# Kernel tuning notes

Hardware: AMD Instinct MI355X
Metric: run time of the kernel (lower is better)

Reference implementation:

```python
import jax, jax.numpy as jnp
import numpy as np

INPUT_DIM = 1024
DAY_EMB = 8
PRED_LEN = 96
HIDDEN = 512
BATCH = 4096


def setup_inputs() -> dict:
    key = jax.random.key(0)
    ks = jax.random.split(key, 6)
    x = jax.random.normal(ks[0], (BATCH, INPUT_DIM), dtype=jnp.float32)
    day_emb = jax.random.normal(ks[1], (PRED_LEN, DAY_EMB), dtype=jnp.float32)
    # stacked per-head first-layer weights: in = input_dim + day_emb_dim
    W1 = jax.random.normal(ks[2], (PRED_LEN, INPUT_DIM + DAY_EMB, HIDDEN), dtype=jnp.float32) * 0.02
    b1 = jax.random.normal(ks[3], (PRED_LEN, HIDDEN), dtype=jnp.float32) * 0.02
    # stacked per-head output Linear(hidden, 1) weights (squeezed)
    W2 = jax.random.normal(ks[4], (PRED_LEN, HIDDEN), dtype=jnp.float32) * 0.02
    b2 = jax.random.normal(ks[5], (PRED_LEN,), dtype=jnp.float32) * 0.02
    return {"x": x, "day_emb": day_emb, "W1": W1, "b1": b1, "W2": W2, "b2": b2}


def reference(x, day_emb, W1, b1, W2, b2):
    # Each head p sees f = concat([x, day_emb[p]]) -> Linear -> ReLU -> (Dropout eval=id) -> Linear(.,1)
    # Split W1 into the x-part and emb-part so we never materialize the [P,B,in+emb] concat.
    W1x = W1[:, :INPUT_DIM, :]          # [P, D, H]
    W1e = W1[:, INPUT_DIM:, :]          # [P, E, H]
    h = jnp.einsum('bd,pdh->pbh', x, W1x)  # [P, B, H]
    h = h + (jnp.einsum('pe,peh->ph', day_emb, W1e) + b1)[:, None, :]
    h = jax.nn.relu(h)
    out = jnp.einsum('pbh,ph->pb', h, W2) + b2[:, None]  # [P, B]
    return out.T  # [B, pred_len]
```

## Files before the change

### kernel.cpp

```cpp
#include <hip/hip_runtime.h>
#include <hip/hip_bf16.h>
#include <stdint.h>

#define INPUT_DIM 1024
#define PRED_LEN 96
#define HIDDEN 512
#define BATCH 4096
#define W1_ROWS 1032

typedef __attribute__((ext_vector_type(8))) short bf16x8;
typedef __attribute__((ext_vector_type(4))) float floatx4;

__device__ __forceinline__ unsigned short f32_to_bf16_rne(float f) {
    union { float f; unsigned int u; } v; v.f = f;
    unsigned int u = v.u;
    unsigned int r = u + 0x7fffu + ((u >> 16) & 1u);
    return (unsigned short)(r >> 16);
}

__device__ __forceinline__ void async_copy16(const void* g, void* l) {
    __builtin_amdgcn_global_load_lds(
        (const __attribute__((address_space(1))) unsigned int*)g,
        (__attribute__((address_space(3))) unsigned int*)l, 16, 0, 0);
}

__global__ void convert_x_kernel(const float* __restrict__ x,
                                 unsigned short* __restrict__ xb) {
    int i = (blockIdx.x * 256 + threadIdx.x) * 4;
    float4 v = *reinterpret_cast<const float4*>(x + i);
    ushort4 o;
    o.x = f32_to_bf16_rne(v.x);
    o.y = f32_to_bf16_rne(v.y);
    o.z = f32_to_bf16_rne(v.z);
    o.w = f32_to_bf16_rne(v.w);
    *reinterpret_cast<ushort4*>(xb + i) = o;
}

__global__ void transpose_w1_kernel(const float* __restrict__ W1,
                                    unsigned short* __restrict__ W1t) {
    __shared__ unsigned short tile[64 * 64];
    int bid = blockIdx.x;
    int nt = bid & 7;
    int kt = (bid >> 3) & 15;
    int p  = bid >> 7;
    int t  = threadIdx.x;
    const float* src = W1 + (size_t)p * W1_ROWS * HIDDEN;
    const int k0 = kt * 64, n0 = nt * 64;

    const int tn = t & 15;
    const int tk = t >> 4;
    float4 v[4];
    #pragma unroll
    for (int i = 0; i < 4; ++i)
        v[i] = *reinterpret_cast<const float4*>(src + (size_t)(k0 + 4 * tk + i) * HIDDEN + n0 + 4 * tn);
    const int slot1 = ((tk >> 2) ^ (tn & 3)) * 16 + (tk & 3) * 4;
    {
        ushort4 w0, w1, w2, w3;
        w0.x = f32_to_bf16_rne(v[0].x); w0.y = f32_to_bf16_rne(v[1].x);
        w0.z = f32_to_bf16_rne(v[2].x); w0.w = f32_to_bf16_rne(v[3].x);
        w1.x = f32_to_bf16_rne(v[0].y); w1.y = f32_to_bf16_rne(v[1].y);
        w1.z = f32_to_bf16_rne(v[2].y); w1.w = f32_to_bf16_rne(v[3].y);
        w2.x = f32_to_bf16_rne(v[0].z); w2.y = f32_to_bf16_rne(v[1].z);
        w2.z = f32_to_bf16_rne(v[2].z); w2.w = f32_to_bf16_rne(v[3].z);
        w3.x = f32_to_bf16_rne(v[0].w); w3.y = f32_to_bf16_rne(v[1].w);
        w3.z = f32_to_bf16_rne(v[2].w); w3.w = f32_to_bf16_rne(v[3].w);
        *reinterpret_cast<ushort4*>(tile + (4 * tn + 0) * 64 + slot1) = w0;
        *reinterpret_cast<ushort4*>(tile + (4 * tn + 1) * 64 + slot1) = w1;
        *reinterpret_cast<ushort4*>(tile + (4 * tn + 2) * 64 + slot1) = w2;
        *reinterpret_cast<ushort4*>(tile + (4 * tn + 3) * 64 + slot1) = w3;
    }
    __syncthreads();

    const int nr = t >> 2;
    const int q  = t & 3;
    const int slot2 = (q ^ ((nr >> 2) & 3)) * 16;
    uint4 a = *reinterpret_cast<const uint4*>(tile + nr * 64 + slot2);
    uint4 b = *reinterpret_cast<const uint4*>(tile + nr * 64 + slot2 + 8);
    size_t dst = ((size_t)p * HIDDEN + n0 + nr) * 1024 + k0 + q * 16;
    *reinterpret_cast<uint4*>(W1t + dst)     = a;
    *reinterpret_cast<uint4*>(W1t + dst + 8) = b;
}

__global__ void bias_kernel(const float* __restrict__ W1,
                            const float* __restrict__ day_emb,
                            const float* __restrict__ b1,
                            float* __restrict__ bias) {
    int p = blockIdx.x;
    int h = threadIdx.x;
    const float* W1e = W1 + ((size_t)p * W1_ROWS + INPUT_DIM) * HIDDEN;
    float acc = b1[p * HIDDEN + h];
    #pragma unroll
    for (int e = 0; e < 8; ++e)
        acc += day_emb[p * 8 + e] * W1e[(size_t)e * HIDDEN + h];
    bias[p * HIDDEN + h] = acc;
}

__global__ void __launch_bounds__(512, 2)
mlp_head_kernel(const unsigned short* __restrict__ xb,
                const unsigned short* __restrict__ W1t,
                const float* __restrict__ bias,
                const float* __restrict__ W2,
                const float* __restrict__ b2,
                float* __restrict__ out)
{
    __shared__ unsigned short A_lds[2][256 * 64];
    __shared__ unsigned short B_lds[2][256 * 64];
    __shared__ float w2s[HIDDEN];
    __shared__ float biass[HIDDEN];
    __shared__ float red[4][256];

    const int mt   = blockIdx.x;
    const int p    = blockIdx.y;
    const int t    = threadIdx.x;
    const int lane = t & 63;
    const int w    = t >> 6;
    const int wm   = w >> 2;
    const int wn   = w & 3;
    const int l15  = lane & 15;
    const int quad = lane >> 4;
    const int sl0  = (quad ^ (l15 & 7)) * 8;
    const int sl1  = ((4 + quad) ^ (l15 & 7)) * 8;

    const int aro = (wm * 128 + l15) * 64;
    const int bro = (wn * 64  + l15) * 64;

    const int tr   = t >> 3;
    const int skc  = ((t & 7) ^ (tr & 7)) * 8;
    const int ldst = t * 8;

    const int m0 = mt * 256;
    const unsigned short* agb = xb  + (size_t)(m0 + tr) * 1024 + skc;
    const unsigned short* bgb = W1t + ((size_t)p * HIDDEN + tr) * 1024 + skc;

    for (int i = t; i < HIDDEN; i += 512) {
        w2s[i]   = W2[p * HIDDEN + i];
        biass[i] = bias[p * HIDDEN + i];
    }
    __syncthreads();

    float partial[8][4];
    #pragma unroll
    for (int i = 0; i < 8; ++i)
        #pragma unroll
        for (int r = 0; r < 4; ++r) partial[i][r] = 0.f;

    for (int nt = 0; nt < 2; ++nt) {
        const size_t bnt = (size_t)nt * 256 * 1024;

        floatx4 acc[8][4];
        #pragma unroll
        for (int i = 0; i < 8; ++i)
            #pragma unroll
            for (int j = 0; j < 4; ++j)
                acc[i][j] = (floatx4){0.f, 0.f, 0.f, 0.f};

        #pragma unroll
        for (int part = 0; part < 4; ++part) {
            async_copy16(agb + (size_t)part * 65536,       &A_lds[0][part * 4096 + ldst]);
            async_copy16(bgb + bnt + (size_t)part * 65536, &B_lds[0][part * 4096 + ldst]);
        }
        asm volatile("s_waitcnt vmcnt(0)" ::: "memory");
        __builtin_amdgcn_s_barrier();

        for (int kt = 0; kt < 16; ++kt) {
            const int cur = kt & 1;
            const unsigned short* Ab = A_lds[cur];
            const unsigned short* Bb = B_lds[cur];
            unsigned short* An = A_lds[cur ^ 1];
            unsigned short* Bn = B_lds[cur ^ 1];
            const int kof = (kt + 1) * 64;
            bf16x8 af[4][2], bf[2][2];

            #pragma unroll
            for (int i = 0; i < 4; ++i) {
                af[i][0] = *reinterpret_cast<const bf16x8*>(Ab + aro + i * 1024 + sl0);
                af[i][1] = *reinterpret_cast<const bf16x8*>(Ab + aro + i * 1024 + sl1);
            }
            #pragma unroll
            for (int j = 0; j < 2; ++j) {
                bf[j][0] = *reinterpret_cast<const bf16x8*>(Bb + bro + j * 1024 + sl0);
                bf[j][1] = *reinterpret_cast<const bf16x8*>(Bb + bro + j * 1024 + sl1);
            }
            if (kt < 15) {
                async_copy16(agb + kof,                &An[ldst]);
                async_copy16(agb + 65536 + kof,        &An[4096 + ldst]);
                async_copy16(bgb + bnt + kof,          &Bn[ldst]);
                async_copy16(bgb + bnt + 65536 + kof,  &Bn[4096 + ldst]);
            }
            __builtin_amdgcn_s_barrier();
            __builtin_amdgcn_s_setprio(1);
            #pragma unroll
            for (int i = 0; i < 4; ++i)
                #pragma unroll
                for (int j = 0; j < 2; ++j) {
                    acc[i][j] = __builtin_amdgcn_mfma_f32_16x16x32_bf16(af[i][0], bf[j][0], acc[i][j], 0, 0, 0);
                    acc[i][j] = __builtin_amdgcn_mfma_f32_16x16x32_bf16(af[i][1], bf[j][1], acc[i][j], 0, 0, 0);
                }
            __builtin_amdgcn_s_setprio(0);
            __builtin_amdgcn_s_barrier();

            #pragma unroll
            for (int j = 0; j < 2; ++j) {
                bf[j][0] = *reinterpret_cast<const bf16x8*>(Bb + bro + (j + 2) * 1024 + sl0);
                bf[j][1] = *reinterpret_cast<const bf16x8*>(Bb + bro + (j + 2) * 1024 + sl1);
            }
            if (kt < 15) {
                async_copy16(agb + 131072 + kof,       &An[8192 + ldst]);
                async_copy16(agb + 196608 + kof,       &An[12288 + ldst]);
                async_copy16(bgb + bnt + 131072 + kof, &Bn[8192 + ldst]);
                async_copy16(bgb + bnt + 196608 + kof, &Bn[12288 + ldst]);
            }
            __builtin_amdgcn_s_barrier();
            __builtin_amdgcn_s_setprio(1);
            #pragma unroll
            for (int i = 0; i < 4; ++i)
                #pragma unroll
                for (int j = 0; j < 2; ++j) {
                    acc[i][j + 2] = __builtin_amdgcn_mfma_f32_16x16x32_bf16(af[i][0], bf[j][0], acc[i][j + 2], 0, 0, 0);
                    acc[i][j + 2] = __builtin_amdgcn_mfma_f32_16x16x32_bf16(af[i][1], bf[j][1], acc[i][j + 2], 0, 0, 0);
                }
            __builtin_amdgcn_s_setprio(0);
            __builtin_amdgcn_s_barrier();

            #pragma unroll
            for (int i = 0; i < 4; ++i) {
                af[i][0] = *reinterpret_cast<const bf16x8*>(Ab + aro + (i + 4) * 1024 + sl0);
                af[i][1] = *reinterpret_cast<const bf16x8*>(Ab + aro + (i + 4) * 1024 + sl1);
            }
            __builtin_amdgcn_s_barrier();
            __builtin_amdgcn_s_setprio(1);
            #pragma unroll
            for (int i = 0; i < 4; ++i)
                #pragma unroll
                for (int j = 0; j < 2; ++j) {
                    acc[i + 4][j + 2] = __builtin_amdgcn_mfma_f32_16x16x32_bf16(af[i][0], bf[j][0], acc[i + 4][j + 2], 0, 0, 0);
                    acc[i + 4][j + 2] = __builtin_amdgcn_mfma_f32_16x16x32_bf16(af[i][1], bf[j][1], acc[i + 4][j + 2], 0, 0, 0);
                }
            __builtin_amdgcn_s_setprio(0);
            __builtin_amdgcn_s_barrier();

            #pragma unroll
            for (int j = 0; j < 2; ++j) {
                bf[j][0] = *reinterpret_cast<const bf16x8*>(Bb + bro + j * 1024 + sl0);
                bf[j][1] = *reinterpret_cast<const bf16x8*>(Bb + bro + j * 1024 + sl1);
            }
            __builtin_amdgcn_s_barrier();
            __builtin_amdgcn_s_setprio(1);
            #pragma unroll
            for (int i = 0; i < 4; ++i)
                #pragma unroll
                for (int j = 0; j < 2; ++j) {
                    acc[i + 4][j] = __builtin_amdgcn_mfma_f32_16x16x32_bf16(af[i][0], bf[j][0], acc[i + 4][j], 0, 0, 0);
                    acc[i + 4][j] = __builtin_amdgcn_mfma_f32_16x16x32_bf16(af[i][1], bf[j][1], acc[i + 4][j], 0, 0, 0);
                }
            __builtin_amdgcn_s_setprio(0);
            if (kt < 15)
                asm volatile("s_waitcnt vmcnt(0)" ::: "memory");
            __builtin_amdgcn_s_barrier();
        }

        const int nb0 = nt * 256;
        #pragma unroll
        for (int j = 0; j < 4; ++j) {
            int c = nb0 + wn * 64 + j * 16 + l15;
            float w2v = w2s[c];
            float bv  = biass[c];
            #pragma unroll
            for (int i = 0; i < 8; ++i)
                #pragma unroll
                for (int r = 0; r < 4; ++r) {
                    float hv = acc[i][j][r] + bv;
                    hv = hv > 0.f ? hv : 0.f;
                    partial[i][r] += hv * w2v;
                }
        }
    }

    #pragma unroll
    for (int i = 0; i < 8; ++i)
        #pragma unroll
        for (int r = 0; r < 4; ++r) {
            float v = partial[i][r];
            v += __shfl_xor(v, 1);
            v += __shfl_xor(v, 2);
            v += __shfl_xor(v, 4);
            v += __shfl_xor(v, 8);
            partial[i][r] = v;
        }

    if (l15 == 0) {
        #pragma unroll
        for (int i = 0; i < 8; ++i)
            #pragma unroll
            for (int r = 0; r < 4; ++r) {
                int row = wm * 128 + i * 16 + quad * 4 + r;
                red[wn][row] = partial[i][r];
            }
    }
    __syncthreads();
    if (t < 256) {
        float v = red[0][t] + red[1][t] + red[2][t] + red[3][t] + b2[p];
        out[(size_t)(m0 + t) * PRED_LEN + p] = v;
    }
}

extern "C" void kernel_launch(void* const* d_in, const int* in_sizes, int n_in,
                              void* d_out, int out_size, void* d_ws, size_t ws_size,
                              hipStream_t stream) {
    const float* x       = (const float*)d_in[0];
    const float* day_emb = (const float*)d_in[1];
    const float* W1      = (const float*)d_in[2];
    const float* b1      = (const float*)d_in[3];
    const float* W2      = (const float*)d_in[4];
    const float* b2      = (const float*)d_in[5];
    float* out = (float*)d_out;

    const size_t xb_bytes  = (size_t)BATCH * INPUT_DIM * 2;
    const size_t w1t_bytes = (size_t)PRED_LEN * HIDDEN * INPUT_DIM * 2;
    const size_t bias_bytes = (size_t)PRED_LEN * HIDDEN * 4;
    if (ws_size < xb_bytes + w1t_bytes + bias_bytes) return;

    unsigned short* xb  = (unsigned short*)d_ws;
    unsigned short* w1t = (unsigned short*)((char*)d_ws + xb_bytes);
    float* biasp        = (float*)((char*)d_ws + xb_bytes + w1t_bytes);

    convert_x_kernel<<<(BATCH * INPUT_DIM) / (256 * 4), 256, 0, stream>>>(x, xb);
    transpose_w1_kernel<<<PRED_LEN * 16 * 8, 256, 0, stream>>>(W1, w1t);
    bias_kernel<<<PRED_LEN, HIDDEN, 0, stream>>>(W1, day_emb, b1, biasp);

    dim3 grid(BATCH / 256, PRED_LEN);
    mlp_head_kernel<<<grid, 512, 0, stream>>>(xb, w1t, biasp, W2, b2, out);
}
```

Before: 676.4 us.

## Halve M tile and use triple-buffered LDS pipeline with fused N-tile loop

Shrinks the per-block M tile from 256 to 128 rows, doubling the grid, and replaces the double-buffered, barrier-heavy K loop with a three-stage ring that prefetches two K-steps ahead and waits with a partial vmcnt. The two N halves are merged into one 32-step virtual loop, and the ReLU/W2 epilogue for the first half runs mid-loop. The intent is fewer barriers, deeper load/compute overlap and better occupancy from lower register use. The cost is more total global traffic for W1 tiles, since each W1 panel is now read by twice as many blocks, and the early w2s/bias __syncthreads is removed, so correctness depends on the loop's barrier ordering those shared writes.

```diff
diff --git a/kernel.cpp b/kernel.cpp
--- a/kernel.cpp
+++ b/kernel.cpp
@@ -103,11 +103,11 @@
                 const float* __restrict__ b2,
                 float* __restrict__ out)
 {
-    __shared__ unsigned short A_lds[2][256 * 64];
-    __shared__ unsigned short B_lds[2][256 * 64];
+    __shared__ unsigned short A_lds[3][128 * 64];
+    __shared__ unsigned short B_lds[3][256 * 64];
     __shared__ float w2s[HIDDEN];
     __shared__ float biass[HIDDEN];
-    __shared__ float red[4][256];
+    __shared__ float red[4][128];
 
     const int mt   = blockIdx.x;
     const int p    = blockIdx.y;
@@ -121,14 +121,14 @@
     const int sl0  = (quad ^ (l15 & 7)) * 8;
     const int sl1  = ((4 + quad) ^ (l15 & 7)) * 8;
 
-    const int aro = (wm * 128 + l15) * 64;
-    const int bro = (wn * 64  + l15) * 64;
+    const int aro = (wm * 64 + l15) * 64;
+    const int bro = (wn * 64 + l15) * 64;
 
     const int tr   = t >> 3;
     const int skc  = ((t & 7) ^ (tr & 7)) * 8;
     const int ldst = t * 8;
 
-    const int m0 = mt * 256;
+    const int m0 = mt * 128;
     const unsigned short* agb = xb  + (size_t)(m0 + tr) * 1024 + skc;
     const unsigned short* bgb = W1t + ((size_t)p * HIDDEN + tr) * 1024 + skc;
 
@@ -136,41 +136,63 @@
         w2s[i]   = W2[p * HIDDEN + i];
         biass[i] = bias[p * HIDDEN + i];
     }
-    __syncthreads();
-
-    float partial[8][4];
-    #pragma unroll
-    for (int i = 0; i < 8; ++i)
+
+    float partial[4][4];
+    #pragma unroll
+    for (int i = 0; i < 4; ++i)
         #pragma unroll
         for (int r = 0; r < 4; ++r) partial[i][r] = 0.f;
 
-    for (int nt = 0; nt < 2; ++nt) {
-        const size_t bnt = (size_t)nt * 256 * 1024;
-
-        floatx4 acc[8][4];
-        #pragma unroll
-        for (int i = 0; i < 8; ++i)
-            #pragma unroll
-            for (int j = 0; j < 4; ++j)
-                acc[i][j] = (floatx4){0.f, 0.f, 0.f, 0.f};
-
-        #pragma unroll
-        for (int part = 0; part < 4; ++part) {
-            async_copy16(agb + (size_t)part * 65536,       &A_lds[0][part * 4096 + ldst]);
-            async_copy16(bgb + bnt + (size_t)part * 65536, &B_lds[0][part * 4096 + ldst]);
-        }
-        asm volatile("s_waitcnt vmcnt(0)" ::: "memory");
+    floatx4 acc[4][4];
+    #pragma unroll
+    for (int i = 0; i < 4; ++i)
+        #pragma unroll
+        for (int j = 0; j < 4; ++j)
+            acc[i][j] = (floatx4){0.f, 0.f, 0.f, 0.f};
+
+    {
+        async_copy16(agb,                 &A_lds[0][ldst]);
+        async_copy16(agb + 65536,         &A_lds[0][4096 + ldst]);
+        async_copy16(bgb,                 &B_lds[0][ldst]);
+        async_copy16(bgb + 65536,         &B_lds[0][4096 + ldst]);
+        async_copy16(bgb + 131072,        &B_lds[0][8192 + ldst]);
+        async_copy16(bgb + 196608,        &B_lds[0][12288 + ldst]);
+        async_copy16(agb + 64,            &A_lds[1][ldst]);
+        async_copy16(agb + 65536 + 64,    &A_lds[1][4096 + ldst]);
+        async_copy16(bgb + 64,            &B_lds[1][ldst]);
+        async_copy16(bgb + 65536 + 64,    &B_lds[1][4096 + ldst]);
+        async_copy16(bgb + 131072 + 64,   &B_lds[1][8192 + ldst]);
+        async_copy16(bgb + 196608 + 64,   &B_lds[1][12288 + ldst]);
+    }
+
+    int cs = 0;
+    int ss = 2;
+
+    #pragma unroll 1
+    for (int vkt = 0; vkt < 31; ++vkt) {
+        asm volatile("s_waitcnt vmcnt(6)" ::: "memory");
         __builtin_amdgcn_s_barrier();
 
-        for (int kt = 0; kt < 16; ++kt) {
-            const int cur = kt & 1;
-            const unsigned short* Ab = A_lds[cur];
-            const unsigned short* Bb = B_lds[cur];
-            unsigned short* An = A_lds[cur ^ 1];
-            unsigned short* Bn = B_lds[cur ^ 1];
-            const int kof = (kt + 1) * 64;
+        if (vkt < 30) {
+            const int v2 = vkt + 2;
+            const int ko = (v2 & 15) << 6;
+            const size_t no = (size_t)(v2 >> 4) * 262144;
+            const unsigned short* a2 = agb + ko;
+            const unsigned short* bq = bgb + no + ko;
+            unsigned short* Ad = &A_lds[ss][ldst];
+            unsigned short* Bd = &B_lds[ss][ldst];
+            async_copy16(a2,           Ad);
+            async_copy16(a2 + 65536,   Ad + 4096);
+            async_copy16(bq,           Bd);
+            async_copy16(bq + 65536,   Bd + 4096);
+            async_copy16(bq + 131072,  Bd + 8192);
+            async_copy16(bq + 196608,  Bd + 12288);
+        }
+
+        {
+            const unsigned short* Ab = &A_lds[cs][0];
+            const unsigned short* Bb = &B_lds[cs][0];
             bf16x8 af[4][2], bf[2][2];
-
             #pragma unroll
             for (int i = 0; i < 4; ++i) {
                 af[i][0] = *reinterpret_cast<const bf16x8*>(Ab + aro + i * 1024 + sl0);
@@ -181,13 +203,6 @@
                 bf[j][0] = *reinterpret_cast<const bf16x8*>(Bb + bro + j * 1024 + sl0);
                 bf[j][1] = *reinterpret_cast<const bf16x8*>(Bb + bro + j * 1024 + sl1);
             }
-            if (kt < 15) {
-                async_copy16(agb + kof,                &An[ldst]);
-                async_copy16(agb + 65536 + kof,        &An[4096 + ldst]);
-                async_copy16(bgb + bnt + kof,          &Bn[ldst]);
-                async_copy16(bgb + bnt + 65536 + kof,  &Bn[4096 + ldst]);
-            }
-            __builtin_amdgcn_s_barrier();
             __builtin_amdgcn_s_setprio(1);
             #pragma unroll
             for (int i = 0; i < 4; ++i)
@@ -197,20 +212,11 @@
                     acc[i][j] = __builtin_amdgcn_mfma_f32_16x16x32_bf16(af[i][1], bf[j][1], acc[i][j], 0, 0, 0);
                 }
             __builtin_amdgcn_s_setprio(0);
-            __builtin_amdgcn_s_barrier();
-
             #pragma unroll
             for (int j = 0; j < 2; ++j) {
                 bf[j][0] = *reinterpret_cast<const bf16x8*>(Bb + bro + (j + 2) * 1024 + sl0);
                 bf[j][1] = *reinterpret_cast<const bf16x8*>(Bb + bro + (j + 2) * 1024 + sl1);
             }
-            if (kt < 15) {
-                async_copy16(agb + 131072 + kof,       &An[8192 + ldst]);
-                async_copy16(agb + 196608 + kof,       &An[12288 + ldst]);
-                async_copy16(bgb + bnt + 131072 + kof, &Bn[8192 + ldst]);
-                async_copy16(bgb + bnt + 196608 + kof, &Bn[12288 + ldst]);
-            }
-            __builtin_amdgcn_s_barrier();
             __builtin_amdgcn_s_setprio(1);
             #pragma unroll
             for (int i = 0; i < 4; ++i)
@@ -220,64 +226,83 @@
                     acc[i][j + 2] = __builtin_amdgcn_mfma_f32_16x16x32_bf16(af[i][1], bf[j][1], acc[i][j + 2], 0, 0, 0);
                 }
             __builtin_amdgcn_s_setprio(0);
-            __builtin_amdgcn_s_barrier();
-
-            #pragma unroll
-            for (int i = 0; i < 4; ++i) {
-                af[i][0] = *reinterpret_cast<const bf16x8*>(Ab + aro + (i + 4) * 1024 + sl0);
-                af[i][1] = *reinterpret_cast<const bf16x8*>(Ab + aro + (i + 4) * 1024 + sl1);
-            }
-            __builtin_amdgcn_s_barrier();
-            __builtin_amdgcn_s_setprio(1);
-            #pragma unroll
-            for (int i = 0; i < 4; ++i)
+        }
+
+        if (vkt == 15) {
+            #pragma unroll
+            for (int j = 0; j < 4; ++j) {
+                int c = wn * 64 + j * 16 + l15;
+                float w2v = w2s[c];
+                float bv  = biass[c];
                 #pragma unroll
-                for (int j = 0; j < 2; ++j) {
-                    acc[i + 4][j + 2] = __builtin_amdgcn_mfma_f32_16x16x32_bf16(af[i][0], bf[j][0], acc[i + 4][j + 2], 0, 0, 0);
-                    acc[i + 4][j + 2] = __builtin_amdgcn_mfma_f32_16x16x32_bf16(af[i][1], bf[j][1], acc[i + 4][j + 2], 0, 0, 0);
-                }
-            __builtin_amdgcn_s_setprio(0);
-            __builtin_amdgcn_s_barrier();
-
+                for (int i = 0; i < 4; ++i)
+                    #pragma unroll
+                    for (int r = 0; r < 4; ++r) {
+                        float hv = acc[i][j][r] + bv;
+                        hv = hv > 0.f ? hv : 0.f;
+                        partial[i][r] += hv * w2v;
+                        acc[i][j][r] = 0.f;
+                    }
+            }
+        }
+
+        cs = (cs == 2) ? 0 : cs + 1;
+        ss = (ss == 2) ? 0 : ss + 1;
+    }
+
+    asm volatile("s_waitcnt vmcnt(0)" ::: "memory");
+    __builtin_amdgcn_s_barrier();
+    {
+        const unsigned short* Ab = &A_lds[1][0];
+        const unsigned short* Bb = &B_lds[1][0];
+        bf16x8 af[4][2], bf[2][2];
+        #pragma unroll
+        for (int i = 0; i < 4; ++i) {
+            af[i][0] = *reinterpret_cast<const bf16x8*>(Ab + aro + i * 1024 + sl0);
+            af[i][1] = *reinterpret_cast<const bf16x8*>(Ab + aro + i * 1024 + sl1);
+        }
+        #pragma unroll
+        for (int j = 0; j < 2; ++j) {
+            bf[j][0] = *reinterpret_cast<const bf16x8*>(Bb + bro + j * 1024 + sl0);
+            bf[j][1] = *reinterpret_cast<const bf16x8*>(Bb + bro + j * 1024 + sl1);
+        }
+        #pragma unroll
+        for (int i = 0; i < 4; ++i)
             #pragma unroll
             for (int j = 0; j < 2; ++j) {
-                bf[j][0] = *reinterpret_cast<const bf16x8*>(Bb + bro + j * 1024 + sl0);
-                bf[j][1] = *reinterpret_cast<const bf16x8*>(Bb + bro + j * 1024 + sl1);
-            }
-            __builtin_amdgcn_s_barrier();
-            __builtin_amdgcn_s_setprio(1);
-            #pragma unroll
-            for (int i = 0; i < 4; ++i)
-                #pragma unroll
-                for (int j = 0; j < 2; ++j) {
-                    acc[i + 4][j] = __builtin_amdgcn_mfma_f32_16x16x32_bf16(af[i][0], bf[j][0], acc[i + 4][j], 0, 0, 0);
-                    acc[i + 4][j] = __builtin_amdgcn_mfma_f32_16x16x32_bf16(af[i][1], bf[j][1], acc[i + 4][j], 0, 0, 0);
-                }
-            __builtin_amdgcn_s_setprio(0);
-            if (kt < 15)
-                asm volatile("s_waitcnt vmcnt(0)" ::: "memory");
-            __builtin_amdgcn_s_barrier();
-        }
-
-        const int nb0 = nt * 256;
-        #pragma unroll
-        for (int j = 0; j < 4; ++j) {
-            int c = nb0 + wn * 64 + j * 16 + l15;
-            float w2v = w2s[c];
-            float bv  = biass[c];
-            #pragma unroll
-            for (int i = 0; i < 8; ++i)
-                #pragma unroll
-                for (int r = 0; r < 4; ++r) {
-                    float hv = acc[i][j][r] + bv;
-                    hv = hv > 0.f ? hv : 0.f;
-                    partial[i][r] += hv * w2v;
-                }
-        }
-    }
-
-    #pragma unroll
-    for (int i = 0; i < 8; ++i)
+                acc[i][j] = __builtin_amdgcn_mfma_f32_16x16x32_bf16(af[i][0], bf[j][0], acc[i][j], 0, 0, 0);
+                acc[i][j] = __builtin_amdgcn_mfma_f32_16x16x32_bf16(af[i][1], bf[j][1], acc[i][j], 0, 0, 0);
+            }
+        #pragma unroll
+        for (int j = 0; j < 2; ++j) {
+            bf[j][0] = *reinterpret_cast<const bf16x8*>(Bb + bro + (j + 2) * 1024 + sl0);
+            bf[j][1] = *reinterpret_cast<const bf16x8*>(Bb + bro + (j + 2) * 1024 + sl1);
+        }
+        #pragma unroll
+        for (int i = 0; i < 4; ++i)
+            #pragma unroll
+            for (int j = 0; j < 2; ++j) {
+                acc[i][j + 2] = __builtin_amdgcn_mfma_f32_16x16x32_bf16(af[i][0], bf[j][0], acc[i][j + 2], 0, 0, 0);
+                acc[i][j + 2] = __builtin_amdgcn_mfma_f32_16x16x32_bf16(af[i][1], bf[j][1], acc[i][j + 2], 0, 0, 0);
+            }
+    }
+    #pragma unroll
+    for (int j = 0; j < 4; ++j) {
+        int c = 256 + wn * 64 + j * 16 + l15;
+        float w2v = w2s[c];
+        float bv  = biass[c];
+        #pragma unroll
+        for (int i = 0; i < 4; ++i)
+            #pragma unroll
+            for (int r = 0; r < 4; ++r) {
+                float hv = acc[i][j][r] + bv;
+                hv = hv > 0.f ? hv : 0.f;
+                partial[i][r] += hv * w2v;
+            }
+    }
+
+    #pragma unroll
+    for (int i = 0; i < 4; ++i)
         #pragma unroll
         for (int r = 0; r < 4; ++r) {
             float v = partial[i][r];
@@ -290,15 +315,15 @@
 
     if (l15 == 0) {
         #pragma unroll
-        for (int i = 0; i < 8; ++i)
+        for (int i = 0; i < 4; ++i)
             #pragma unroll
             for (int r = 0; r < 4; ++r) {
-                int row = wm * 128 + i * 16 + quad * 4 + r;
+                int row = wm * 64 + i * 16 + quad * 4 + r;
                 red[wn][row] = partial[i][r];
             }
     }
     __syncthreads();
-    if (t < 256) {
+    if (t < 128) {
         float v = red[0][t] + red[1][t] + red[2][t] + red[3][t] + b2[p];
         out[(size_t)(m0 + t) * PRED_LEN + p] = v;
     }
@@ -328,6 +353,6 @@
     transpose_w1_kernel<<<PRED_LEN * 16 * 8, 256, 0, stream>>>(W1, w1t);
     bias_kernel<<<PRED_LEN, HIDDEN, 0, stream>>>(W1, day_emb, b1, biasp);
 
-    dim3 grid(BATCH / 256, PRED_LEN);
+    dim3 grid(BATCH / 128, PRED_LEN);
     mlp_head_kernel<<<grid, 512, 0, stream>>>(xb, w1t, biasp, W2, b2, out);
 }
```

After: 824.0 us. +21.8%, slower.
